# Kernel tuning notes

Measured on AMD Instinct MI355X. Metric: run time of the kernel, lower is better.

Reference implementation:

```python
import jax, jax.numpy as jnp
import numpy as np

DIM = 512
HEADS = 8
DIM_HEAD = 64
HIDDEN = HEADS * DIM_HEAD  # 512
SCALE = DIM_HEAD ** -0.5
EPS = 1e-5


def setup_inputs() -> dict:
    key = jax.random.key(0)
    ks = jax.random.split(key, 6)
    B, N = 4, 8192
    x = jax.random.normal(ks[0], (B, DIM, N), dtype=jnp.float32)
    ln_w = jnp.ones((DIM,), dtype=jnp.float32)
    ln_b = jnp.zeros((DIM,), dtype=jnp.float32)
    # stored as (in, out) so y = x @ W
    w_qkv = jax.random.normal(ks[1], (DIM, 3 * HIDDEN), dtype=jnp.float32) * (DIM ** -0.5)
    w_out = jax.random.normal(ks[2], (HIDDEN, DIM), dtype=jnp.float32) * (HIDDEN ** -0.5)
    b_out = jnp.zeros((DIM,), dtype=jnp.float32)
    return {"x": x, "ln_w": ln_w, "ln_b": ln_b, "w_qkv": w_qkv, "w_out": w_out, "b_out": b_out}


def _forward(x, ln_w, ln_b, w_qkv, w_out, b_out):
    B, D, N = x.shape
    h = jnp.swapaxes(x, 1, 2)  # b n d
    # LayerNorm over last dim
    mu = jnp.mean(h, axis=-1, keepdims=True)
    var = jnp.var(h, axis=-1, keepdims=True)
    h = (h - mu) * jax.lax.rsqrt(var + EPS) * ln_w + ln_b
    qkv = h @ w_qkv  # b n 3*hidden
    q, k, v = jnp.split(qkv, 3, axis=-1)
    # b n (h d) -> b h n d
    reshape = lambda t: jnp.swapaxes(t.reshape(B, N, HEADS, DIM_HEAD), 1, 2)
    q, k, v = reshape(q), reshape(k), reshape(v)
    q = jax.nn.softmax(q * SCALE, axis=-2)  # softmax over tokens n
    k = jax.nn.softmax(k, axis=-1)          # softmax over features d
    context = jnp.einsum('bhnd,bhne->bhde', k, v)  # small d x e per head
    out = jnp.einsum('bhde,bhnd->bhen', context, q)
    # b h e n -> b n (h e)
    out = jnp.swapaxes(out, 1, 3).reshape(B, N, HIDDEN)  # bhen -> bneh? careful: need (h e)
    # redo correctly: bhen -> b n h e -> b n (h e)
    # (the line above gives b n e h; compute properly instead)
    return out


def reference(x, ln_w, ln_b, w_qkv, w_out, b_out):
    B, D, N = x.shape
    h = jnp.swapaxes(x, 1, 2)  # b n d
    mu = jnp.mean(h, axis=-1, keepdims=True)
    var = jnp.var(h, axis=-1, keepdims=True)
    h = (h - mu) * jax.lax.rsqrt(var + EPS) * ln_w + ln_b
    qkv = h @ w_qkv  # b n 3*hidden
    q, k, v = jnp.split(qkv, 3, axis=-1)
    reshape = lambda t: jnp.swapaxes(t.reshape(B, N, HEADS, DIM_HEAD), 1, 2)  # b h n d
    q, k, v = reshape(q), reshape(k), reshape(v)
    q = jax.nn.softmax(q * SCALE, axis=-2)  # over tokens
    k = jax.nn.softmax(k, axis=-1)          # over head-dim
    context = jnp.einsum('bhnd,bhne->bhde', k, v)
    out = jnp.einsum('bhde,bhnd->bnhe', context, q)  # b n h e
    out = out.reshape(B, N, HIDDEN)  # (h e) concatenated per head
    out = out @ w_out + b_out  # b n dim
    return jnp.swapaxes(out, 1, 2)  # b dim n
```

## Files before the change

### kernel.cpp

```cpp
#include <hip/hip_runtime.h>

#define B_   4
#define N_   8192
#define D_   512
#define NH   8
#define DH   64
#define HID  512

typedef unsigned short u16;
typedef __attribute__((ext_vector_type(8))) short  bf16x8;
typedef __attribute__((ext_vector_type(8))) unsigned short u16x8;
typedef __attribute__((ext_vector_type(4))) float  f32x4;

__device__ __forceinline__ float bf2f(u16 u) {
  unsigned int i = ((unsigned int)u) << 16;
  return __builtin_bit_cast(float, i);
}
__device__ __forceinline__ u16 f2bf(float f) {
  unsigned int i = __builtin_bit_cast(unsigned int, f);
  i += 0x7fff + ((i >> 16) & 1);
  return (u16)(i >> 16);
}

#define GLOAD16(g, l) \
  __builtin_amdgcn_global_load_lds((const __attribute__((address_space(1))) void*)(g), \
                                   (__attribute__((address_space(3))) void*)(l), 16, 0, 0)

__global__ __launch_bounds__(256) void transpose_f2b(const float* __restrict__ in,
                                                     u16* __restrict__ out,
                                                     int rows, int cols) {
  __shared__ u16 tile[64][65];
  int c0 = blockIdx.x * 64, r0 = blockIdx.y * 64;
  int t = threadIdx.x;
  int rl = t >> 6, cl = t & 63;
#pragma unroll
  for (int i = 0; i < 16; i++) {
    int r = i * 4 + rl;
    tile[r][cl] = f2bf(in[(long)(r0 + r) * cols + c0 + cl]);
  }
  __syncthreads();
  int c4 = t >> 6, rr = t & 63;
#pragma unroll
  for (int i = 0; i < 16; i++) {
    int c = i * 4 + c4;
    out[(long)(c0 + c) * rows + r0 + rr] = tile[rr][c];
  }
}

__global__ __launch_bounds__(256) void ln_kernel(const float* __restrict__ x,
                                                 const float* __restrict__ lw,
                                                 const float* __restrict__ lb,
                                                 u16* __restrict__ h) {
  __shared__ u16 xs[32 * 520];
  __shared__ float red[2][8][32];
  __shared__ float murs[2][32];
  __shared__ float lws[512], lbs[512];
  int b = blockIdx.y, n0 = blockIdx.x * 32;
  int t = threadIdx.x;
  lws[t] = lw[t]; lws[t + 256] = lw[t + 256];
  lbs[t] = lb[t]; lbs[t + 256] = lb[t + 256];
  int tok = t & 31, dp = t >> 5;
  const float* xp = x + (long)b * D_ * N_ + n0 + tok;
  float s = 0.f, s2 = 0.f;
#pragma unroll 8
  for (int i = 0; i < 64; i++) {
    int d = dp * 64 + i;
    float v = xp[(long)d * N_];
    s += v; s2 += v * v;
    xs[tok * 520 + d] = f2bf(v);
  }
  red[0][dp][tok] = s; red[1][dp][tok] = s2;
  __syncthreads();
  if (t < 32) {
    float S1 = 0.f, S2 = 0.f;
#pragma unroll
    for (int i = 0; i < 8; i++) { S1 += red[0][i][t]; S2 += red[1][i][t]; }
    float mu = S1 * (1.0f / 512.0f);
    float var = S2 * (1.0f / 512.0f) - mu * mu;
    murs[0][t] = mu; murs[1][t] = rsqrtf(var + 1e-5f);
  }
  __syncthreads();
  int row = t >> 3, seg = t & 7;
  float mu = murs[0][row], rs = murs[1][row];
  u16* hp = h + ((long)b * N_ + n0 + row) * D_;
  const u16* xr = xs + row * 520;
#pragma unroll
  for (int c = 0; c < 8; c++) {
    int d0 = c * 64 + seg * 8;
    u16x8 in8 = *(const u16x8*)(xr + d0);
    u16x8 o;
#pragma unroll
    for (int i = 0; i < 8; i++) {
      int d = d0 + i;
      o[i] = f2bf((bf2f(in8[i]) - mu) * rs * lws[d] + lbs[d]);
    }
    *(u16x8*)(hp + d0) = o;
  }
}

__global__ __launch_bounds__(256) void gemm1(const u16* __restrict__ A,
                                             const u16* __restrict__ B,
                                             u16* __restrict__ qexp,
                                             u16* __restrict__ expkT,
                                             u16* __restrict__ vT,
                                             float* __restrict__ S,
                                             float* __restrict__ Z) {
  const int K = 512;
  __shared__ alignas(16) u16 smem[17408];

  int bid = blockIdx.y * 12 + blockIdx.x;
  int wid = (bid & 7) * 384 + (bid >> 3);
  int bx = wid % 12, by = wid / 12;
  int m0 = by * 128, n0 = bx * 128;

  int tid = threadIdx.x, wave = tid >> 6, lane = tid & 63;
  int l15 = lane & 15, qd = lane >> 4;

  int ra0 = tid >> 2,          qa0 = (tid & 3) ^ ((ra0 >> 1) & 3);
  int ra1 = (tid + 256) >> 2,  qa1 = (tid & 3) ^ ((ra1 >> 1) & 3);
  const u16* gA0 = A + (long)(m0 + ra0) * K + qa0 * 8;
  const u16* gA1 = A + (long)(m0 + ra1) * K + qa1 * 8;
  const u16* gB0 = B + (long)(n0 + ra0) * K + qa0 * 8;
  const u16* gB1 = B + (long)(n0 + ra1) * K + qa1 * 8;

  int wm = wave & 1, wn = wave >> 1;
  int aoff[4], boff[4];
#pragma unroll
  for (int i = 0; i < 4; i++) {
    int r = wm * 64 + i * 16 + l15;
    aoff[i] = r * 32 + ((qd ^ ((r >> 1) & 3)) * 8);
    int rb = wn * 64 + i * 16 + l15;
    boff[i] = rb * 32 + ((qd ^ ((rb >> 1) & 3)) * 8);
  }

  f32x4 zero = {0.f, 0.f, 0.f, 0.f};
  f32x4 acc[4][4];
#pragma unroll
  for (int i = 0; i < 4; i++)
#pragma unroll
    for (int j = 0; j < 4; j++) acc[i][j] = zero;

#define STAGE1(buf, kk) { \
    u16* dA = smem + (buf) * 8192 + wave * 512; \
    u16* dB = smem + (buf) * 8192 + 4096 + wave * 512; \
    GLOAD16(gA0 + (kk), dA); GLOAD16(gA1 + (kk), dA + 2048); \
    GLOAD16(gB0 + (kk), dB); GLOAD16(gB1 + (kk), dB + 2048); }

  STAGE1(0, 0);
  asm volatile("s_waitcnt vmcnt(0)" ::: "memory");
  __builtin_amdgcn_s_barrier();

#pragma unroll
  for (int it = 0; it < 15; it++) {
    const int cur = it & 1, nxt = cur ^ 1;
    STAGE1(nxt, (it + 1) * 32);
    const u16* Ac = smem + cur * 8192;
    const u16* Bc = smem + cur * 8192 + 4096;
    bf16x8 af[4], bf[4];
#pragma unroll
    for (int q = 0; q < 4; q++) {
      af[q] = *(const bf16x8*)(Ac + aoff[q]);
      bf[q] = *(const bf16x8*)(Bc + boff[q]);
    }
#pragma unroll
    for (int i = 0; i < 4; i++)
#pragma unroll
      for (int j = 0; j < 4; j++)
        acc[i][j] = __builtin_amdgcn_mfma_f32_16x16x32_bf16(af[i], bf[j], acc[i][j], 0, 0, 0);
    asm volatile("s_waitcnt vmcnt(0) lgkmcnt(0)" ::: "memory");
    __builtin_amdgcn_s_barrier();
  }
  {
    const u16* Ac = smem + 8192;
    const u16* Bc = smem + 8192 + 4096;
    bf16x8 af[4], bf[4];
#pragma unroll
    for (int q = 0; q < 4; q++) {
      af[q] = *(const bf16x8*)(Ac + aoff[q]);
      bf[q] = *(const bf16x8*)(Bc + boff[q]);
    }
#pragma unroll
    for (int i = 0; i < 4; i++)
#pragma unroll
      for (int j = 0; j < 4; j++)
        acc[i][j] = __builtin_amdgcn_mfma_f32_16x16x32_bf16(af[i], bf[j], acc[i][j], 0, 0, 0);
  }
  asm volatile("s_waitcnt lgkmcnt(0)" ::: "memory");
  __builtin_amdgcn_s_barrier();
#undef STAGE1

  u16* Cs = smem;

  int third = n0 >> 9;
  int n0t = n0 & 511;
  int b = m0 >> 13;
  int tloc = m0 & 8191;

  if (third == 0) {
#pragma unroll
    for (int i = 0; i < 4; i++)
#pragma unroll
      for (int j = 0; j < 4; j++)
#pragma unroll
        for (int r = 0; r < 4; r++) acc[i][j][r] = __expf(acc[i][j][r] * 0.125f);
#pragma unroll
    for (int j = 0; j < 4; j++) {
      float ps = 0.f;
#pragma unroll
      for (int i = 0; i < 4; i++)
#pragma unroll
        for (int r = 0; r < 4; r++) ps += acc[i][j][r];
      ps += __shfl_xor(ps, 16);
      ps += __shfl_xor(ps, 32);
      if (qd == 0) atomicAdd(S + b * 512 + n0t + wn * 64 + j * 16 + l15, ps);
    }
  } else if (third == 1) {
#pragma unroll
    for (int i = 0; i < 4; i++)
#pragma unroll
      for (int j = 0; j < 4; j++)
#pragma unroll
        for (int r = 0; r < 4; r++) acc[i][j][r] = __expf(acc[i][j][r]);
    int head = (n0t >> 6) + wn;
#pragma unroll
    for (int i = 0; i < 4; i++)
#pragma unroll
      for (int r = 0; r < 4; r++) {
        float rs = acc[i][0][r] + acc[i][1][r] + acc[i][2][r] + acc[i][3][r];
        rs += __shfl_xor(rs, 1);
        rs += __shfl_xor(rs, 2);
        rs += __shfl_xor(rs, 4);
        rs += __shfl_xor(rs, 8);
        if (l15 == 0)
          atomicAdd(Z + ((long)b * NH + head) * 8192 + tloc + wm * 64 + i * 16 + qd * 4 + r, rs);
      }
  }

  if (third == 0) {
#pragma unroll
    for (int i = 0; i < 4; i++)
#pragma unroll
      for (int r = 0; r < 4; r++)
#pragma unroll
        for (int j = 0; j < 4; j++)
          Cs[(wm * 64 + i * 16 + qd * 4 + r) * 136 + wn * 64 + j * 16 + l15] =
              f2bf(acc[i][j][r]);
  } else {
#pragma unroll
    for (int i = 0; i < 4; i++)
#pragma unroll
      for (int r = 0; r < 4; r++)
#pragma unroll
        for (int j = 0; j < 4; j++)
          Cs[(wn * 64 + j * 16 + l15) * 136 + wm * 64 + i * 16 + qd * 4 + r] =
              f2bf(acc[i][j][r]);
  }
  __syncthreads();

  u16* dst; long ldg;
  if (third == 0)      { dst = qexp  + ((long)b * N_ + tloc) * 512 + n0t;  ldg = 512; }
  else if (third == 1) { dst = expkT + ((long)b * 512 + n0t) * 8192 + tloc; ldg = 8192; }
  else                 { dst = vT    + ((long)b * 512 + n0t) * 8192 + tloc; ldg = 8192; }

  int seg = lane & 7;
#pragma unroll
  for (int outer = 0; outer < 2; outer++)
#pragma unroll
    for (int rr = 0; rr < 2; rr++) {
      int row = outer * 64 + wave * 16 + rr * 8 + (lane >> 3);
      const u16* src = Cs + row * 136;
      u16* dp = dst + (long)row * ldg;
#pragma unroll
      for (int p = 0; p < 2; p++)
        *(uint4*)(dp + p * 64 + seg * 8) = *(const uint4*)(src + p * 64 + seg * 8);
    }
}

__global__ __launch_bounds__(256) void zrecip(float* __restrict__ Z) {
  int i = blockIdx.x * 256 + threadIdx.x;
  Z[i] = 1.0f / Z[i];
}

__global__ __launch_bounds__(256) void ctx_kernel(const u16* __restrict__ expkT,
                                                  const u16* __restrict__ vT,
                                                  const float* __restrict__ Zr,
                                                  float* __restrict__ ctx) {
  __shared__ u16 As[64 * 128];
  __shared__ u16 Bs[64 * 128];
  int kc = blockIdx.x, hh = blockIdx.y, b = blockIdx.z;
  int t = threadIdx.x, w = t >> 6, l = t & 63, l15 = l & 15, qd = l >> 4;
  long nbase = (long)kc * 512;
  const u16* Abase = expkT + ((long)b * 512 + hh * 64) * 8192 + nbase;
  const u16* Bbase = vT   + ((long)b * 512 + hh * 64) * 8192 + nbase;
  const float* Zb = Zr + ((long)b * NH + hh) * 8192 + nbase;

  f32x4 zero = {0.f, 0.f, 0.f, 0.f};
  f32x4 acc[4] = {zero, zero, zero, zero};

  int brow = t >> 2;
  for (int s = 0; s < 4; s++) {
    long ko = (long)s * 128;
    __syncthreads();
#pragma unroll
    for (int si = 0; si < 4; si++) {
      int qq = si * 4 + w;
      int row = qq * 4 + (l >> 4);
      int gs = (l & 15) ^ (row & 15);
      GLOAD16(Abase + (long)row * 8192 + ko + gs * 8, As + qq * 512);
    }
    {
      const u16* src = Bbase + (long)brow * 8192 + ko;
#pragma unroll
      for (int cc = 0; cc < 4; cc++) {
        int c = (t & 3) * 4 + cc;
        u16x8 v8 = *(const u16x8*)(src + c * 8);
        float4 z0 = *(const float4*)(Zb + ko + c * 8);
        float4 z1 = *(const float4*)(Zb + ko + c * 8 + 4);
        u16x8 o;
        o[0] = f2bf(bf2f(v8[0]) * z0.x); o[1] = f2bf(bf2f(v8[1]) * z0.y);
        o[2] = f2bf(bf2f(v8[2]) * z0.z); o[3] = f2bf(bf2f(v8[3]) * z0.w);
        o[4] = f2bf(bf2f(v8[4]) * z1.x); o[5] = f2bf(bf2f(v8[5]) * z1.y);
        o[6] = f2bf(bf2f(v8[6]) * z1.z); o[7] = f2bf(bf2f(v8[7]) * z1.w);
        *(u16x8*)(Bs + brow * 128 + ((c ^ (brow & 15)) * 8)) = o;
      }
    }
    __syncthreads();
#pragma unroll
    for (int kk = 0; kk < 4; kk++) {
      int ar = w * 16 + l15;
      bf16x8 af = *(const bf16x8*)(As + ar * 128 + (((kk * 4 + qd) ^ (ar & 15)) * 8));
#pragma unroll
      for (int j = 0; j < 4; j++) {
        int br = j * 16 + l15;
        bf16x8 bf8 = *(const bf16x8*)(Bs + br * 128 + (((kk * 4 + qd) ^ (br & 15)) * 8));
        acc[j] = __builtin_amdgcn_mfma_f32_16x16x32_bf16(af, bf8, acc[j], 0, 0, 0);
      }
    }
  }
  float* cp = ctx + ((long)(b * NH + hh)) * DH * DH;
#pragma unroll
  for (int j = 0; j < 4; j++)
#pragma unroll
    for (int r = 0; r < 4; r++)
      atomicAdd(cp + (w * 16 + qd * 4 + r) * 64 + j * 16 + l15, acc[j][r]);
}

__global__ __launch_bounds__(256) void mprime(const float* __restrict__ ctx,
                                              const float* __restrict__ wout,
                                              const float* __restrict__ S,
                                              u16* __restrict__ Mt) {
  __shared__ float ws[64 * 65];
  __shared__ float cs[64 * 65];
  int dt = blockIdx.x, hh = blockIdx.y, b = blockIdx.z;
  int t = threadIdx.x;
  {
    int e = t >> 2;
#pragma unroll
    for (int ii = 0; ii < 4; ii++) {
      int col = (t & 3) * 16 + ii * 4;
      float4 v = *(const float4*)(wout + (long)(hh * 64 + e) * 512 + dt * 64 + col);
      ws[e * 65 + col] = v.x; ws[e * 65 + col + 1] = v.y;
      ws[e * 65 + col + 2] = v.z; ws[e * 65 + col + 3] = v.w;
      float4 c = *(const float4*)(ctx + ((long)(b * NH + hh)) * 4096 + (long)e * 64 + col);
      cs[e * 65 + col] = c.x; cs[e * 65 + col + 1] = c.y;
      cs[e * 65 + col + 2] = c.z; cs[e * 65 + col + 3] = c.w;
    }
  }
  __syncthreads();
  int dol = t & 63, dg = t >> 6;
#pragma unroll
  for (int dd = 0; dd < 16; dd++) {
    int d = dg * 16 + dd;
    float v = 0.f;
#pragma unroll 8
    for (int e = 0; e < 64; e++) v += cs[d * 65 + e] * ws[e * 65 + dol];
    float sv = S[b * 512 + hh * 64 + d];
    Mt[(long)b * 262144 + (long)(dt * 64 + dol) * 512 + hh * 64 + d] = f2bf(v / sv);
  }
}

__global__ __launch_bounds__(256) void gemm_tn_f(const u16* __restrict__ A,
                                                 const u16* __restrict__ B,
                                                 float* __restrict__ C,
                                                 const float* __restrict__ bias,
                                                 int K, int ldc,
                                                 long sA, long sB, long sC) {
  __shared__ alignas(16) u16 smem[17408];
  float* Cf = (float*)smem;

  int bid = (blockIdx.z * gridDim.y + blockIdx.y) * gridDim.x + blockIdx.x;
  int wid = (bid & 7) * 128 + (bid >> 3);
  int mx = wid & 3;
  int ny = (wid >> 2) & 63;
  long bz = wid >> 8;
  A += bz * sA; B += bz * sB; C += bz * sC;
  int m0 = mx * 128, n0 = ny * 128;

  int tid = threadIdx.x, wave = tid >> 6, lane = tid & 63;
  int l15 = lane & 15, qd = lane >> 4;

  int ra0 = tid >> 2,          qa0 = (tid & 3) ^ ((ra0 >> 1) & 3);
  int ra1 = (tid + 256) >> 2,  qa1 = (tid & 3) ^ ((ra1 >> 1) & 3);
  const u16* gA0 = A + (long)(m0 + ra0) * K + qa0 * 8;
  const u16* gA1 = A + (long)(m0 + ra1) * K + qa1 * 8;
  const u16* gB0 = B + (long)(n0 + ra0) * K + qa0 * 8;
  const u16* gB1 = B + (long)(n0 + ra1) * K + qa1 * 8;

  int wm = wave & 1, wn = wave >> 1;
  int aoff[4], boff[4];
#pragma unroll
  for (int i = 0; i < 4; i++) {
    int r = wm * 64 + i * 16 + l15;
    aoff[i] = r * 32 + ((qd ^ ((r >> 1) & 3)) * 8);
    int rb = wn * 64 + i * 16 + l15;
    boff[i] = rb * 32 + ((qd ^ ((rb >> 1) & 3)) * 8);
  }

  f32x4 zero = {0.f, 0.f, 0.f, 0.f};
  f32x4 acc[4][4];
#pragma unroll
  for (int i = 0; i < 4; i++)
#pragma unroll
    for (int j = 0; j < 4; j++) acc[i][j] = zero;

#define STAGE2(buf, kk) { \
    u16* dA = smem + (buf) * 8192 + wave * 512; \
    u16* dB = smem + (buf) * 8192 + 4096 + wave * 512; \
    GLOAD16(gA0 + (kk), dA); GLOAD16(gA1 + (kk), dA + 2048); \
    GLOAD16(gB0 + (kk), dB); GLOAD16(gB1 + (kk), dB + 2048); }

  STAGE2(0, 0);
  asm volatile("s_waitcnt vmcnt(0)" ::: "memory");
  __builtin_amdgcn_s_barrier();

#pragma unroll
  for (int it = 0; it < 15; it++) {
    const int cur = it & 1, nxt = cur ^ 1;
    STAGE2(nxt, (it + 1) * 32);
    const u16* Ac = smem + cur * 8192;
    const u16* Bc = smem + cur * 8192 + 4096;
    bf16x8 af[4], bf[4];
#pragma unroll
    for (int q = 0; q < 4; q++) {
      af[q] = *(const bf16x8*)(Ac + aoff[q]);
      bf[q] = *(const bf16x8*)(Bc + boff[q]);
    }
#pragma unroll
    for (int i = 0; i < 4; i++)
#pragma unroll
      for (int j = 0; j < 4; j++)
        acc[i][j] = __builtin_amdgcn_mfma_f32_16x16x32_bf16(af[i], bf[j], acc[i][j], 0, 0, 0);
    asm volatile("s_waitcnt vmcnt(0) lgkmcnt(0)" ::: "memory");
    __builtin_amdgcn_s_barrier();
  }
  {
    const u16* Ac = smem + 8192;
    const u16* Bc = smem + 8192 + 4096;
    bf16x8 af[4], bf[4];
#pragma unroll
    for (int q = 0; q < 4; q++) {
      af[q] = *(const bf16x8*)(Ac + aoff[q]);
      bf[q] = *(const bf16x8*)(Bc + boff[q]);
    }
#pragma unroll
    for (int i = 0; i < 4; i++)
#pragma unroll
      for (int j = 0; j < 4; j++)
        acc[i][j] = __builtin_amdgcn_mfma_f32_16x16x32_bf16(af[i], bf[j], acc[i][j], 0, 0, 0);
  }
  asm volatile("s_waitcnt lgkmcnt(0)" ::: "memory");
  __builtin_amdgcn_s_barrier();
#undef STAGE2

#pragma unroll
  for (int half = 0; half < 2; half++) {
    __syncthreads();
    if (wm == half) {
#pragma unroll
      for (int i = 0; i < 4; i++)
#pragma unroll
        for (int r = 0; r < 4; r++) {
          int rl = i * 16 + qd * 4 + r;
          float bv = bias[m0 + half * 64 + rl];
#pragma unroll
          for (int j = 0; j < 4; j++)
            Cf[rl * 133 + wn * 64 + j * 16 + l15] = acc[i][j][r] + bv;
        }
    }
    __syncthreads();
#pragma unroll
    for (int z = 0; z < 2; z++) {
      int rl = z * 32 + (tid >> 3);
      int seg = tid & 7;
      float* dp = C + (long)(m0 + half * 64 + rl) * ldc + n0;
      const float* src = Cf + rl * 133;
#pragma unroll
      for (int p = 0; p < 4; p++)
        *(float4*)(dp + p * 32 + seg * 4) = *(const float4*)(src + p * 32 + seg * 4);
    }
  }
}

extern "C" void kernel_launch(void* const* d_in, const int* in_sizes, int n_in,
                              void* d_out, int out_size, void* d_ws, size_t ws_size,
                              hipStream_t stream) {
  const float* x    = (const float*)d_in[0];
  const float* lnw  = (const float*)d_in[1];
  const float* lnb  = (const float*)d_in[2];
  const float* wqkv = (const float*)d_in[3];
  const float* wout = (const float*)d_in[4];
  const float* bout = (const float*)d_in[5];
  float* out = (float*)d_out;
  char* ws = (char*)d_ws;

  u16*  h     = (u16*)(ws + 0L);
  u16*  qexp  = (u16*)(ws + 33554432L);
  u16*  expkT = (u16*)(ws + 67108864L);
  u16*  vT    = (u16*)(ws + 100663296L);
  u16*  wqkvT = (u16*)(ws + 134217728L);
  u16*  Mt    = (u16*)(ws + 134217728L);
  float* S    = (float*)(ws + 136314880L);
  float* ctx  = (float*)(ws + 0L);
  float* Z    = (float*)d_out;

  hipMemsetAsync(S, 0, 4 * 512 * 4, stream);
  hipMemsetAsync(Z, 0, (long)B_ * NH * 8192 * 4, stream);

  transpose_f2b<<<dim3(24, 8), 256, 0, stream>>>(wqkv, wqkvT, 512, 1536);

  ln_kernel<<<dim3(256, 4), 256, 0, stream>>>(x, lnw, lnb, h);

  gemm1<<<dim3(12, 256), 256, 0, stream>>>(h, wqkvT, qexp, expkT, vT, S, Z);

  zrecip<<<dim3(1024), 256, 0, stream>>>(Z);

  hipMemsetAsync(ctx, 0, 4 * 8 * 64 * 64 * 4, stream);

  ctx_kernel<<<dim3(16, 8, 4), 256, 0, stream>>>(expkT, vT, Z, ctx);

  mprime<<<dim3(8, 8, 4), 256, 0, stream>>>(ctx, wout, S, Mt);

  gemm_tn_f<<<dim3(4, 64, 4), 256, 0, stream>>>(Mt, qexp, out, bout, 512, 8192,
                                                262144L, (long)8192 * 512, (long)512 * 8192);
}
```

Measured before the change: 286.8 us.

## Enlarge QKV GEMM tile to 256x256 with 8 waves and interleaved prefetch

The QKV projection GEMM moves from 128x128 tiles with 4 waves to 256x256 tiles with 8 waves, using a 64-wide K step with XOR-swizzled LDS and split A/B prefetch interleaved between MFMA phases. It also adds s_setprio around the MFMA blocks, and the epilogue writes out in two halves through LDS. The aim is more data reuse per global load, fewer K iterations and barriers, and better overlap of loads with compute. In exchange it uses far more LDS and registers (an 8x4 accumulator array per wave), which lowers occupancy, and it launches only 768 blocks, which may hurt tail balance.

```diff
diff --git a/kernel.cpp b/kernel.cpp
--- a/kernel.cpp
+++ b/kernel.cpp
@@ -98,98 +98,126 @@
   }
 }
 
-__global__ __launch_bounds__(256) void gemm1(const u16* __restrict__ A,
-                                             const u16* __restrict__ B,
-                                             u16* __restrict__ qexp,
-                                             u16* __restrict__ expkT,
-                                             u16* __restrict__ vT,
-                                             float* __restrict__ S,
-                                             float* __restrict__ Z) {
-  const int K = 512;
-  __shared__ alignas(16) u16 smem[17408];
-
-  int bid = blockIdx.y * 12 + blockIdx.x;
-  int wid = (bid & 7) * 384 + (bid >> 3);
-  int bx = wid % 12, by = wid / 12;
-  int m0 = by * 128, n0 = bx * 128;
-
-  int tid = threadIdx.x, wave = tid >> 6, lane = tid & 63;
+__global__ __launch_bounds__(512, 2) void gemm1(const u16* __restrict__ A,
+                                                const u16* __restrict__ B,
+                                                u16* __restrict__ qexp,
+                                                u16* __restrict__ expkT,
+                                                u16* __restrict__ vT,
+                                                float* __restrict__ S,
+                                                float* __restrict__ Z) {
+  __shared__ alignas(16) u16 smem[65536];
+
+  int bid = blockIdx.y * 6 + blockIdx.x;
+  int wid = (bid & 7) * 96 + (bid >> 3);
+  int bx = wid % 6, by = wid / 6;
+  int m0 = by * 256, n0 = bx * 256;
+
+  int tid = threadIdx.x, w = tid >> 6, lane = tid & 63;
   int l15 = lane & 15, qd = lane >> 4;
-
-  int ra0 = tid >> 2,          qa0 = (tid & 3) ^ ((ra0 >> 1) & 3);
-  int ra1 = (tid + 256) >> 2,  qa1 = (tid & 3) ^ ((ra1 >> 1) & 3);
-  const u16* gA0 = A + (long)(m0 + ra0) * K + qa0 * 8;
-  const u16* gA1 = A + (long)(m0 + ra1) * K + qa1 * 8;
-  const u16* gB0 = B + (long)(n0 + ra0) * K + qa0 * 8;
-  const u16* gB1 = B + (long)(n0 + ra1) * K + qa1 * 8;
-
-  int wm = wave & 1, wn = wave >> 1;
-  int aoff[4], boff[4];
-#pragma unroll
-  for (int i = 0; i < 4; i++) {
-    int r = wm * 64 + i * 16 + l15;
-    aoff[i] = r * 32 + ((qd ^ ((r >> 1) & 3)) * 8);
-    int rb = wn * 64 + i * 16 + l15;
-    boff[i] = rb * 32 + ((qd ^ ((rb >> 1) & 3)) * 8);
-  }
+  int wm = w >> 2, wn = w & 3;
+
+  int rl = lane >> 3;
+  int sg8 = ((lane & 7) ^ rl) * 8;
+  int ofsA[2][2], ofsB[2][2];
+#pragma unroll
+  for (int q = 0; q < 2; q++)
+#pragma unroll
+    for (int hs = 0; hs < 2; hs++) {
+      int r = hs * 128 + (w * 2 + q) * 8 + rl;
+      ofsA[q][hs] = (m0 + r) * 512;
+      ofsB[q][hs] = (n0 + r) * 512;
+    }
+  const u16* Ag = A + sg8;
+  const u16* Bg = B + sg8;
+
+  int baseA = (wm * 128 + l15) * 64 + ((qd ^ (l15 & 7)) * 8);
+  int baseB = (wn * 64 + l15) * 64 + ((qd ^ (l15 & 7)) * 8);
 
   f32x4 zero = {0.f, 0.f, 0.f, 0.f};
-  f32x4 acc[4][4];
-#pragma unroll
-  for (int i = 0; i < 4; i++)
+  f32x4 acc[8][4];
+#pragma unroll
+  for (int i = 0; i < 8; i++)
 #pragma unroll
     for (int j = 0; j < 4; j++) acc[i][j] = zero;
 
-#define STAGE1(buf, kk) { \
-    u16* dA = smem + (buf) * 8192 + wave * 512; \
-    u16* dB = smem + (buf) * 8192 + 4096 + wave * 512; \
-    GLOAD16(gA0 + (kk), dA); GLOAD16(gA1 + (kk), dA + 2048); \
-    GLOAD16(gB0 + (kk), dB); GLOAD16(gB1 + (kk), dB + 2048); }
-
-  STAGE1(0, 0);
-  asm volatile("s_waitcnt vmcnt(0)" ::: "memory");
+#define STG_A(buf, hs, kt) { \
+    GLOAD16(Ag + ofsA[0][hs] + (kt) * 64, smem + (buf) * 16384 + (hs) * 8192 + (w * 2 + 0) * 512); \
+    GLOAD16(Ag + ofsA[1][hs] + (kt) * 64, smem + (buf) * 16384 + (hs) * 8192 + (w * 2 + 1) * 512); }
+#define STG_B(buf, hs, kt) { \
+    GLOAD16(Bg + ofsB[0][hs] + (kt) * 64, smem + 32768 + (buf) * 16384 + (hs) * 8192 + (w * 2 + 0) * 512); \
+    GLOAD16(Bg + ofsB[1][hs] + (kt) * 64, smem + 32768 + (buf) * 16384 + (hs) * 8192 + (w * 2 + 1) * 512); }
+
+  STG_A(0, 0, 0); STG_A(0, 1, 0);
+  STG_B(0, 0, 0); STG_B(0, 1, 0);
+  STG_A(1, 0, 1); STG_A(1, 1, 1);
+  asm volatile("s_waitcnt vmcnt(4)" ::: "memory");
   __builtin_amdgcn_s_barrier();
 
 #pragma unroll
-  for (int it = 0; it < 15; it++) {
-    const int cur = it & 1, nxt = cur ^ 1;
-    STAGE1(nxt, (it + 1) * 32);
-    const u16* Ac = smem + cur * 8192;
-    const u16* Bc = smem + cur * 8192 + 4096;
-    bf16x8 af[4], bf[4];
-#pragma unroll
-    for (int q = 0; q < 4; q++) {
-      af[q] = *(const bf16x8*)(Ac + aoff[q]);
-      bf[q] = *(const bf16x8*)(Bc + boff[q]);
-    }
-#pragma unroll
-    for (int i = 0; i < 4; i++)
-#pragma unroll
-      for (int j = 0; j < 4; j++)
-        acc[i][j] = __builtin_amdgcn_mfma_f32_16x16x32_bf16(af[i], bf[j], acc[i][j], 0, 0, 0);
-    asm volatile("s_waitcnt vmcnt(0) lgkmcnt(0)" ::: "memory");
+  for (int tt = 0; tt < 8; tt++) {
+    const int c = tt & 1;
+    const u16* Ab = smem + c * 16384;
+    const u16* Bb = smem + 32768 + c * 16384;
+    bf16x8 aL[4][2], aH[4][2], bb[4][2];
+#pragma unroll
+    for (int i = 0; i < 4; i++)
+#pragma unroll
+      for (int ks = 0; ks < 2; ks++)
+        aL[i][ks] = *(const bf16x8*)(Ab + ((baseA + i * 1024) ^ (ks * 32)));
+#pragma unroll
+    for (int j = 0; j < 4; j++)
+#pragma unroll
+      for (int ks = 0; ks < 2; ks++)
+        bb[j][ks] = *(const bf16x8*)(Bb + ((baseB + j * 1024) ^ (ks * 32)));
+    __builtin_amdgcn_s_setprio(1);
+#pragma unroll
+    for (int i = 0; i < 4; i++)
+#pragma unroll
+      for (int j = 0; j < 2; j++)
+#pragma unroll
+        for (int ks = 0; ks < 2; ks++)
+          acc[i][j] = __builtin_amdgcn_mfma_f32_16x16x32_bf16(aL[i][ks], bb[j][ks], acc[i][j], 0, 0, 0);
+    __builtin_amdgcn_s_setprio(0);
     __builtin_amdgcn_s_barrier();
-  }
-  {
-    const u16* Ac = smem + 8192;
-    const u16* Bc = smem + 8192 + 4096;
-    bf16x8 af[4], bf[4];
-#pragma unroll
-    for (int q = 0; q < 4; q++) {
-      af[q] = *(const bf16x8*)(Ac + aoff[q]);
-      bf[q] = *(const bf16x8*)(Bc + boff[q]);
-    }
-#pragma unroll
-    for (int i = 0; i < 4; i++)
-#pragma unroll
-      for (int j = 0; j < 4; j++)
-        acc[i][j] = __builtin_amdgcn_mfma_f32_16x16x32_bf16(af[i], bf[j], acc[i][j], 0, 0, 0);
-  }
-  asm volatile("s_waitcnt lgkmcnt(0)" ::: "memory");
-  __builtin_amdgcn_s_barrier();
-#undef STAGE1
-
-  u16* Cs = smem;
+#pragma unroll
+    for (int i = 0; i < 4; i++)
+#pragma unroll
+      for (int ks = 0; ks < 2; ks++)
+        aH[i][ks] = *(const bf16x8*)(Ab + ((baseA + (4 + i) * 1024) ^ (ks * 32)));
+    if (tt < 7) { STG_B(c ^ 1, 0, tt + 1); STG_B(c ^ 1, 1, tt + 1); }
+    __builtin_amdgcn_s_setprio(1);
+#pragma unroll
+    for (int i = 0; i < 4; i++)
+#pragma unroll
+      for (int j = 0; j < 2; j++)
+#pragma unroll
+        for (int ks = 0; ks < 2; ks++)
+          acc[4 + i][j] = __builtin_amdgcn_mfma_f32_16x16x32_bf16(aH[i][ks], bb[j][ks], acc[4 + i][j], 0, 0, 0);
+    __builtin_amdgcn_s_setprio(0);
+    __builtin_amdgcn_s_barrier();
+    if (tt < 6) { STG_A(c, 0, tt + 2); STG_A(c, 1, tt + 2); }
+    __builtin_amdgcn_s_setprio(1);
+#pragma unroll
+    for (int i = 0; i < 4; i++)
+#pragma unroll
+      for (int j = 2; j < 4; j++)
+#pragma unroll
+        for (int ks = 0; ks < 2; ks++)
+          acc[i][j] = __builtin_amdgcn_mfma_f32_16x16x32_bf16(aL[i][ks], bb[j][ks], acc[i][j], 0, 0, 0);
+#pragma unroll
+    for (int i = 0; i < 4; i++)
+#pragma unroll
+      for (int j = 2; j < 4; j++)
+#pragma unroll
+        for (int ks = 0; ks < 2; ks++)
+          acc[4 + i][j] = __builtin_amdgcn_mfma_f32_16x16x32_bf16(aH[i][ks], bb[j][ks], acc[4 + i][j], 0, 0, 0);
+    __builtin_amdgcn_s_setprio(0);
+    if (tt < 6) { asm volatile("s_waitcnt vmcnt(4)" ::: "memory"); }
+    else        { asm volatile("s_waitcnt vmcnt(0)" ::: "memory"); }
+    __builtin_amdgcn_s_barrier();
+  }
+#undef STG_A
+#undef STG_B
 
   int third = n0 >> 9;
   int n0t = n0 & 511;
@@ -198,7 +226,7 @@
 
   if (third == 0) {
 #pragma unroll
-    for (int i = 0; i < 4; i++)
+    for (int i = 0; i < 8; i++)
 #pragma unroll
       for (int j = 0; j < 4; j++)
 #pragma unroll
@@ -207,7 +235,7 @@
     for (int j = 0; j < 4; j++) {
       float ps = 0.f;
 #pragma unroll
-      for (int i = 0; i < 4; i++)
+      for (int i = 0; i < 8; i++)
 #pragma unroll
         for (int r = 0; r < 4; r++) ps += acc[i][j][r];
       ps += __shfl_xor(ps, 16);
@@ -216,14 +244,14 @@
     }
   } else if (third == 1) {
 #pragma unroll
-    for (int i = 0; i < 4; i++)
+    for (int i = 0; i < 8; i++)
 #pragma unroll
       for (int j = 0; j < 4; j++)
 #pragma unroll
         for (int r = 0; r < 4; r++) acc[i][j][r] = __expf(acc[i][j][r]);
     int head = (n0t >> 6) + wn;
 #pragma unroll
-    for (int i = 0; i < 4; i++)
+    for (int i = 0; i < 8; i++)
 #pragma unroll
       for (int r = 0; r < 4; r++) {
         float rs = acc[i][0][r] + acc[i][1][r] + acc[i][2][r] + acc[i][3][r];
@@ -232,48 +260,57 @@
         rs += __shfl_xor(rs, 4);
         rs += __shfl_xor(rs, 8);
         if (l15 == 0)
-          atomicAdd(Z + ((long)b * NH + head) * 8192 + tloc + wm * 64 + i * 16 + qd * 4 + r, rs);
-      }
-  }
-
+          atomicAdd(Z + ((long)b * NH + head) * 8192 + tloc + wm * 128 + i * 16 + qd * 4 + r, rs);
+      }
+  }
+
+  u16* Cs = smem;
   if (third == 0) {
-#pragma unroll
-    for (int i = 0; i < 4; i++)
-#pragma unroll
-      for (int r = 0; r < 4; r++)
-#pragma unroll
-        for (int j = 0; j < 4; j++)
-          Cs[(wm * 64 + i * 16 + qd * 4 + r) * 136 + wn * 64 + j * 16 + l15] =
-              f2bf(acc[i][j][r]);
+    u16* dstb = qexp + ((long)b * 8192 + tloc) * 512 + n0t;
+#pragma unroll
+    for (int hh = 0; hh < 2; hh++) {
+      if (hh) __syncthreads();
+      if (wm == hh) {
+#pragma unroll
+        for (int i = 0; i < 8; i++)
+#pragma unroll
+          for (int r = 0; r < 4; r++)
+#pragma unroll
+            for (int j = 0; j < 4; j++)
+              Cs[(i * 16 + qd * 4 + r) * 264 + wn * 64 + j * 16 + l15] = f2bf(acc[i][j][r]);
+      }
+      __syncthreads();
+      u16* dst = dstb + (long)hh * 128 * 512;
+#pragma unroll
+      for (int z = 0; z < 8; z++) {
+        int row = z * 16 + (tid >> 5);
+        int off = (tid & 31) * 8;
+        *(uint4*)(dst + (long)row * 512 + off) = *(const uint4*)(Cs + row * 264 + off);
+      }
+    }
   } else {
-#pragma unroll
-    for (int i = 0; i < 4; i++)
-#pragma unroll
-      for (int r = 0; r < 4; r++)
-#pragma unroll
-        for (int j = 0; j < 4; j++)
-          Cs[(wn * 64 + j * 16 + l15) * 136 + wm * 64 + i * 16 + qd * 4 + r] =
-              f2bf(acc[i][j][r]);
-  }
-  __syncthreads();
-
-  u16* dst; long ldg;
-  if (third == 0)      { dst = qexp  + ((long)b * N_ + tloc) * 512 + n0t;  ldg = 512; }
-  else if (third == 1) { dst = expkT + ((long)b * 512 + n0t) * 8192 + tloc; ldg = 8192; }
-  else                 { dst = vT    + ((long)b * 512 + n0t) * 8192 + tloc; ldg = 8192; }
-
-  int seg = lane & 7;
-#pragma unroll
-  for (int outer = 0; outer < 2; outer++)
-#pragma unroll
-    for (int rr = 0; rr < 2; rr++) {
-      int row = outer * 64 + wave * 16 + rr * 8 + (lane >> 3);
-      const u16* src = Cs + row * 136;
-      u16* dp = dst + (long)row * ldg;
-#pragma unroll
-      for (int p = 0; p < 2; p++)
-        *(uint4*)(dp + p * 64 + seg * 8) = *(const uint4*)(src + p * 64 + seg * 8);
-    }
+    u16* dstb = (third == 1 ? expkT : vT) + ((long)b * 512 + n0t) * 8192 + tloc;
+#pragma unroll
+    for (int hh = 0; hh < 2; hh++) {
+      if (hh) __syncthreads();
+      if (wm == hh) {
+#pragma unroll
+        for (int i = 0; i < 8; i++)
+#pragma unroll
+          for (int r = 0; r < 4; r++)
+#pragma unroll
+            for (int j = 0; j < 4; j++)
+              Cs[(wn * 64 + j * 16 + l15) * 136 + i * 16 + qd * 4 + r] = f2bf(acc[i][j][r]);
+      }
+      __syncthreads();
+#pragma unroll
+      for (int z = 0; z < 8; z++) {
+        int col = z * 32 + (tid >> 4);
+        int moff = (tid & 15) * 8;
+        *(uint4*)(dstb + (long)col * 8192 + hh * 128 + moff) = *(const uint4*)(Cs + col * 136 + moff);
+      }
+    }
+  }
 }
 
 __global__ __launch_bounds__(256) void zrecip(float* __restrict__ Z) {
@@ -480,20 +517,20 @@
       for (int i = 0; i < 4; i++)
 #pragma unroll
         for (int r = 0; r < 4; r++) {
-          int rl = i * 16 + qd * 4 + r;
-          float bv = bias[m0 + half * 64 + rl];
+          int rrl = i * 16 + qd * 4 + r;
+          float bv = bias[m0 + half * 64 + rrl];
 #pragma unroll
           for (int j = 0; j < 4; j++)
-            Cf[rl * 133 + wn * 64 + j * 16 + l15] = acc[i][j][r] + bv;
+            Cf[rrl * 133 + wn * 64 + j * 16 + l15] = acc[i][j][r] + bv;
         }
     }
     __syncthreads();
 #pragma unroll
     for (int z = 0; z < 2; z++) {
-      int rl = z * 32 + (tid >> 3);
+      int rrl = z * 32 + (tid >> 3);
       int seg = tid & 7;
-      float* dp = C + (long)(m0 + half * 64 + rl) * ldc + n0;
-      const float* src = Cf + rl * 133;
+      float* dp = C + (long)(m0 + half * 64 + rrl) * ldc + n0;
+      const float* src = Cf + rrl * 133;
 #pragma unroll
       for (int p = 0; p < 4; p++)
         *(float4*)(dp + p * 32 + seg * 4) = *(const float4*)(src + p * 32 + seg * 4);
@@ -530,7 +567,7 @@
 
   ln_kernel<<<dim3(256, 4), 256, 0, stream>>>(x, lnw, lnb, h);
 
-  gemm1<<<dim3(12, 256), 256, 0, stream>>>(h, wqkvT, qexp, expkT, vT, S, Z);
+  gemm1<<<dim3(6, 128), 512, 0, stream>>>(h, wqkvT, qexp, expkT, vT, S, Z);
 
   zrecip<<<dim3(1024), 256, 0, stream>>>(Z);
 
```

After: 326.4 us. +13.8%, slower.
